# Kernel optimization log

Hardware: AMD Instinct MI355X
Metric: run time of the kernel (lower is better)

## Reference

```python
import jax, jax.numpy as jnp
import numpy as np

N_NODES = 20000
IN_CH = 7
HID = 256
HEADS = 8
NEG_SLOPE = 0.2


def glorot(key, shape):
    fan = shape[0] + shape[-1] if len(shape) == 2 else int(np.prod(shape))
    lim = jnp.sqrt(6.0 / fan)
    return jax.random.uniform(key, shape, jnp.float32, -lim, lim)


def setup_inputs() -> dict:
    key = jax.random.key(0)
    ks = jax.random.split(key, 12)
    x = jax.random.normal(ks[0], (N_NODES, IN_CH), jnp.float32)
    edge_index = jax.random.randint(ks[1], (2, 160000), 0, N_NODES, jnp.int64)
    # conv1: in=7 -> heads=8, out=256, concat
    W1 = glorot(ks[2], (IN_CH, HEADS * HID))
    att_src1 = glorot(ks[3], (HEADS, HID))
    att_dst1 = glorot(ks[4], (HEADS, HID))
    b1 = jnp.zeros((HEADS * HID,), jnp.float32)
    # conv2: in=2048 -> heads=1, out=256, mean (concat=False)
    W2 = glorot(ks[5], (HEADS * HID, 1 * HID))
    att_src2 = glorot(ks[6], (1, HID))
    att_dst2 = glorot(ks[7], (1, HID))
    b2 = jnp.zeros((HID,), jnp.float32)
    return {"x": x, "edge_index": edge_index, "W1": W1, "att_src1": att_src1,
            "att_dst1": att_dst1, "b1": b1, "W2": W2, "att_src2": att_src2,
            "att_dst2": att_dst2, "b2": b2}


def gat_conv(x, src, dst, W, att_src, att_dst, bias, concat):
    # PyG GATConv (eval mode, dropout disabled)
    H, C = att_src.shape
    n = x.shape[0]
    h = (x @ W).reshape(n, H, C)                      # [N,H,C]
    a_src = jnp.sum(h * att_src[None], axis=-1)       # [N,H]
    a_dst = jnp.sum(h * att_dst[None], axis=-1)       # [N,H]
    alpha = a_src[src] + a_dst[dst]                   # [E,H]
    alpha = jax.nn.leaky_relu(alpha, NEG_SLOPE)
    # segment softmax over incoming edges of each destination node
    amax = jax.ops.segment_max(alpha, dst, num_segments=n)
    alpha = jnp.exp(alpha - amax[dst])
    denom = jax.ops.segment_sum(alpha, dst, num_segments=n)
    alpha = alpha / (denom[dst] + 1e-16)
    msg = h[src] * alpha[:, :, None]                  # [E,H,C] gather + weight
    out = jax.ops.segment_sum(msg, dst, num_segments=n)  # scatter-add aggregate
    out = out.reshape(n, H * C) if concat else out.mean(axis=1)
    return out + bias


def reference(x, edge_index, W1, att_src1, att_dst1, b1, W2, att_src2, att_dst2, b2):
    n = x.shape[0]
    # PyG GATConv default: add self-loops
    loops = jnp.arange(n, dtype=edge_index.dtype)
    src = jnp.concatenate([edge_index[0], loops])
    dst = jnp.concatenate([edge_index[1], loops])
    h = gat_conv(x, src, dst, W1, att_src1, att_dst1, b1, concat=True)
    h = jax.nn.elu(h)
    out = gat_conv(h, src, dst, W2, att_src2, att_dst2, b2, concat=False)
    return out
```

## Files before the change

kernel.cpp:

```cpp
#include <hip/hip_runtime.h>
#include <hip/hip_bf16.h>

#define N_NODES 20000
#define E_ORIG  160000
#define E_TOT   180000
#define HEADS   8
#define HID     256
#define F1      2048
#define NEG     0.2f
#define MAXDEG  96
#define GBKS    32
#define BMG     80

typedef __attribute__((ext_vector_type(8))) short  short8;
typedef __attribute__((ext_vector_type(4))) short  short4_;
typedef __attribute__((ext_vector_type(4))) float  f32x4;

__device__ inline float bf2f(ushort u){ union{unsigned u32; float f;} v; v.u32=((unsigned)u)<<16; return v.f; }
__device__ inline ushort f2bf(float f){
  union{float f; unsigned u;} v; v.f=f;
  unsigned lsb=(v.u>>16)&1u; v.u += 0x7fffu + lsb; return (ushort)(v.u>>16);
}

__device__ inline void gload16(const ushort* g, ushort* s){
  __builtin_amdgcn_global_load_lds((const __attribute__((address_space(1))) unsigned int*)g,
                                   (__attribute__((address_space(3))) unsigned int*)s, 16, 0, 0);
}

__global__ __launch_bounds__(256) void k_pre(const float* __restrict__ x, const float* __restrict__ W1,
    const float* __restrict__ as1, const float* __restrict__ ad1, const float* __restrict__ W2,
    float* __restrict__ a_src1, float* __restrict__ a_dst1, ushort* __restrict__ W2bT,
    int* __restrict__ cnt){
  __shared__ float s_w[128];
  __shared__ ushort sh[256][65];
  int tid = threadIdx.x, bid = blockIdx.x;
  if (tid < 128){
    int t = tid & 63;
    int k = t>>3, i = t&7;
    float v = 0.f;
    if (i < 7){
      const float* wp = W1 + i*F1 + (k<<8);
      const float* ap = ((tid<64) ? as1 : ad1) + (k<<8);
      f32x4 a4 = {0,0,0,0};
      for (int c=0;c<256;c+=4)
        a4 += (*(const f32x4*)&wp[c]) * (*(const f32x4*)&ap[c]);
      v = a4[0]+a4[1]+a4[2]+a4[3];
    }
    s_w[tid] = v;
  }
  __syncthreads();
  {
    int nl = tid>>3, k = tid&7;
    int n = bid*32 + nl;
    if (n < N_NODES){
      float s=0.f, d=0.f;
      const float* ws = &s_w[k*8];
      const float* wd = &s_w[64+k*8];
#pragma unroll
      for (int i=0;i<7;i++){
        float xv = x[n*7+i];
        s += xv*ws[i]; d += xv*wd[i];
      }
      a_src1[n*8+k]=s; a_dst1[n*8+k]=d;
    }
  }
  if (bid >= 32 && bid < 111){
    int i = (bid-32)*256 + tid;
    if (i < N_NODES) cnt[i] = 0;
  }
  if (bid < 32){
    int k0 = bid*64;
    for (int kk=0; kk<64; kk++) sh[tid][kk] = f2bf(W2[(size_t)(k0+kk)*256 + tid]);
    __syncthreads();
#pragma unroll
    for (int c8=0; c8<8; c8++){
      short8 v;
#pragma unroll
      for (int j=0;j<8;j++) v[j] = (short)sh[tid][c8*8+j];
      *(short8*)&W2bT[(size_t)tid*F1 + k0 + c8*8] = v;
    }
  }
}

__global__ void k_scat(const int* __restrict__ ei, int* __restrict__ cnt, int* __restrict__ bucket){
  int e = blockIdx.x*256 + threadIdx.x;
  if (e >= E_TOT) return;
  int s, d;
  if (e < E_ORIG){ s = ei[e]; d = ei[E_ORIG + e]; }
  else           { s = d = e - E_ORIG; }
  int pos = atomicAdd(&cnt[d], 1);
  if (pos < MAXDEG) bucket[d*MAXDEG + pos] = s;
}

__global__ __launch_bounds__(512) void k_sa1(const int* __restrict__ cnt, const int* __restrict__ bucket,
    const float* __restrict__ a_src1, const float* __restrict__ a_dst1,
    const float* __restrict__ x, const float* __restrict__ W1, const float* __restrict__ b1,
    ushort* __restrict__ x2){
  __shared__ float sxa[8][64];
  int tid = threadIdx.x, wv = tid>>6, lane = tid&63;
  int n = blockIdx.x*8 + wv;
  {
    int k = lane>>3, i = lane&7;
    int ie = (i==7)?0:i;
    int base = n*MAXDEG;
    int deg  = cnt[n]; if (deg>MAXDEG) deg=MAXDEG;
    float ad = a_dst1[n*8+k];
    int src0 = (lane<deg)    ? bucket[base+lane]    : 0;
    int src1 = (lane+64<deg) ? bucket[base+lane+64] : 0;
    float denom = 0.f, acc = 0.f;
    int j = 0;
    for (; j+2<=deg; j+=2){
      int s0 = (j<64)   ? __shfl(src0,j)     : __shfl(src1,j-64);
      int s1 = (j+1<64) ? __shfl(src0,j+1)   : __shfl(src1,j-63);
      float A0 = a_src1[(size_t)s0*8+k] + ad;
      float A1 = a_src1[(size_t)s1*8+k] + ad;
      float X0 = x[(size_t)s0*7+ie];
      float X1 = x[(size_t)s1*7+ie];
      A0 = (A0>0.f)?A0:NEG*A0;  A1 = (A1>0.f)?A1:NEG*A1;
      float w0 = __expf(A0),   w1 = __expf(A1);
      denom += w0; acc += w0*X0;
      denom += w1; acc += w1*X1;
    }
    if (j<deg){
      int s0 = (j<64) ? __shfl(src0,j) : __shfl(src1,j-64);
      float A0 = a_src1[(size_t)s0*8+k] + ad;
      A0 = (A0>0.f)?A0:NEG*A0;
      float w0 = __expf(A0);
      denom += w0; acc += w0*x[(size_t)s0*7+ie];
    }
    sxa[wv][lane] = acc/denom;
  }
  __syncthreads();
  int kh = tid>>6, c4 = (tid&63)<<2;
  f32x4 w1r[7];
#pragma unroll
  for (int i=0;i<7;i++) w1r[i] = *(const f32x4*)(W1 + i*F1 + (kh<<8) + c4);
  f32x4 bb = *(const f32x4*)(b1 + (kh<<8) + c4);
#pragma unroll
  for (int g=0; g<8; g++){
    int nn = blockIdx.x*8 + g;
    const float* xa = &sxa[g][kh<<3];
    f32x4 h = bb;
#pragma unroll
    for (int i=0;i<7;i++) h += xa[i]*w1r[i];
    short4_ o;
#pragma unroll
    for (int j=0;j<4;j++){ float v=h[j]; v=(v>0.f)?v:(__expf(v)-1.f); o[j]=(short)f2bf(v); }
    *(short4_*)(x2 + (size_t)nn*F1 + (kh<<8) + c4) = o;
  }
}

__global__ __launch_bounds__(256) void k_gemm2m(const ushort* __restrict__ A,
    const ushort* __restrict__ BT, ushort* __restrict__ h2b,
    const float* __restrict__ as2, const float* __restrict__ ad2,
    float* __restrict__ a_src2, float* __restrict__ a_dst2){
  __shared__ __align__(16) ushort S[2][(BMG+256)*64];
  int tid = threadIdx.x;
  int m0 = blockIdx.x*BMG;
  int w = tid>>6, l = tid&63;
  int lrow = l&15, lk = l>>4;
  int nc = w<<6;

  const ushort* gp[11];
#pragma unroll
  for (int rep=0;rep<11;rep++){
    int lin = rep*256 + tid;
    if (lin < BMG*8){
      int r = lin>>3, s = lin&7;
      gp[rep] = A + (size_t)(m0+r)*F1 + ((s ^ (r&7))<<3);
    } else if (lin < (BMG+256)*8){
      int j = lin - BMG*8;
      int c = j>>3, s = j&7;
      gp[rep] = BT + (size_t)c*F1 + ((s ^ (c&7))<<3);
    } else gp[rep] = BT;
  }

  f32x4 acc[5][4] = {};

#pragma unroll
  for (int rep=0;rep<10;rep++) gload16(gp[rep], &S[0][(rep*256+tid)<<3]);
  if (tid < 128) gload16(gp[10], &S[0][(10*256+tid)<<3]);
  __syncthreads();

  int cur = 0;
  for (int t=0; t<GBKS; t++){
    if (t+1 < GBKS){
      int k0 = (t+1)<<6;
#pragma unroll
      for (int rep=0;rep<10;rep++) gload16(gp[rep]+k0, &S[cur^1][(rep*256+tid)<<3]);
      if (tid < 128) gload16(gp[10]+k0, &S[cur^1][(10*256+tid)<<3]);
    }
    const ushort* as_ = &S[cur][0];
    const ushort* bs_ = &S[cur][BMG*64];
#pragma unroll
    for (int kk=0;kk<2;kk++){
      short8 af[5], bfr[4];
#pragma unroll
      for (int m=0;m<5;m++){
        int r = (m<<4) + lrow;
        af[m] = *(const short8*)&as_[(r<<6) + ((((kk<<2)|lk) ^ (r&7))<<3)];
      }
#pragma unroll
      for (int n=0;n<4;n++){
        int c = nc + (n<<4) + lrow;
        bfr[n] = *(const short8*)&bs_[(c<<6) + ((((kk<<2)|lk) ^ (c&7))<<3)];
      }
#pragma unroll
      for (int m=0;m<5;m++)
#pragma unroll
        for (int n=0;n<4;n++)
          acc[m][n] = __builtin_amdgcn_mfma_f32_16x16x32_bf16(af[m], bfr[n], acc[m][n], 0,0,0);
    }
    __syncthreads();
    cur ^= 1;
  }

  float* sps = (float*)&S[0][0];
  float* spd = sps + BMG*4;
  float s2v[4], d2v[4];
#pragma unroll
  for (int n=0;n<4;n++){
    int col = nc + (n<<4) + lrow;
    s2v[n]=as2[col]; d2v[n]=ad2[col];
  }
#pragma unroll
  for (int m=0;m<5;m++){
#pragma unroll
    for (int j=0;j<4;j++){
      int lr = (m<<4) + (lk<<2) + j;
      int grow = m0 + lr;
      float ps=0.f, pd=0.f;
#pragma unroll
      for (int n=0;n<4;n++){
        float v = acc[m][n][j];
        ps += v*s2v[n]; pd += v*d2v[n];
        h2b[(size_t)grow*256 + nc+(n<<4)+lrow] = f2bf(v);
      }
      ps += __shfl_xor(ps,8); ps += __shfl_xor(ps,4); ps += __shfl_xor(ps,2); ps += __shfl_xor(ps,1);
      pd += __shfl_xor(pd,8); pd += __shfl_xor(pd,4); pd += __shfl_xor(pd,2); pd += __shfl_xor(pd,1);
      if (lrow==0){
        sps[(lr<<2) | w] = ps;
        spd[(lr<<2) | w] = pd;
      }
    }
  }
  __syncthreads();
  if (tid < BMG){
    int grow = m0 + tid;
    f32x4 a = *(const f32x4*)&sps[tid<<2];
    f32x4 b = *(const f32x4*)&spd[tid<<2];
    a_src2[grow] = a[0]+a[1]+a[2]+a[3];
    a_dst2[grow] = b[0]+b[1]+b[2]+b[3];
  }
}

__global__ __launch_bounds__(256) void k_agg2(const int* __restrict__ cnt, const int* __restrict__ bucket,
    const float* __restrict__ a_src2, const float* __restrict__ a_dst2, const ushort* __restrict__ h2b,
    const float* __restrict__ b2, float* __restrict__ out){
  int tid = threadIdx.x, wv = tid>>6, lane = tid&63;
  int n = blockIdx.x*4 + wv;
  int base = n*MAXDEG;
  int deg  = cnt[n]; if (deg > MAXDEG) deg = MAXDEG;
  float ad = a_dst2[n];

  int src0 = (lane<deg)     ? bucket[base+lane]    : 0;
  int src1 = (lane+64<deg)  ? bucket[base+lane+64] : 0;
  float a0 = -1e30f, a1 = -1e30f;
  if (lane<deg)   { float a = a_src2[src0]+ad; a0 = (a>0.f)?a:NEG*a; }
  if (lane+64<deg){ float a = a_src2[src1]+ad; a1 = (a>0.f)?a:NEG*a; }
  float m = fmaxf(a0,a1);
  for (int off=32; off; off>>=1) m = fmaxf(m, __shfl_xor(m,off));
  float e0 = (lane<deg)    ? __expf(a0-m) : 0.f;
  float e1 = (lane+64<deg) ? __expf(a1-m) : 0.f;
  float s = e0+e1;
  for (int off=32; off; off>>=1) s += __shfl_xor(s,off);
  float inv = 1.f/(s+1e-16f);
  e0 *= inv; e1 *= inv;

  int c0 = lane<<2;
  float acc0=0.f, acc1=0.f, acc2=0.f, acc3=0.f;
  int d1 = (deg<64)?deg:64;
  for (int j=0;j<d1;j++){
    float w = __shfl(e0, j);
    int  sj = __shfl(src0, j);
    short4_ hv = *(const short4_*)(h2b + (size_t)sj*256 + c0);
    acc0 += w*bf2f((ushort)hv[0]); acc1 += w*bf2f((ushort)hv[1]);
    acc2 += w*bf2f((ushort)hv[2]); acc3 += w*bf2f((ushort)hv[3]);
  }
  for (int j=64;j<deg;j++){
    float w = __shfl(e1, j-64);
    int  sj = __shfl(src1, j-64);
    short4_ hv = *(const short4_*)(h2b + (size_t)sj*256 + c0);
    acc0 += w*bf2f((ushort)hv[0]); acc1 += w*bf2f((ushort)hv[1]);
    acc2 += w*bf2f((ushort)hv[2]); acc3 += w*bf2f((ushort)hv[3]);
  }
  f32x4 bb = *(const f32x4*)(b2 + c0);
  f32x4 o; o[0]=acc0+bb[0]; o[1]=acc1+bb[1]; o[2]=acc2+bb[2]; o[3]=acc3+bb[3];
  *(f32x4*)(out + (size_t)n*256 + c0) = o;
}

extern "C" void kernel_launch(void* const* d_in, const int* in_sizes, int n_in,
                              void* d_out, int out_size, void* d_ws, size_t ws_size,
                              hipStream_t stream){
  const float* x      = (const float*)d_in[0];
  const int*   ei     = (const int*)  d_in[1];
  const float* W1     = (const float*)d_in[2];
  const float* att_s1 = (const float*)d_in[3];
  const float* att_d1 = (const float*)d_in[4];
  const float* b1     = (const float*)d_in[5];
  const float* W2     = (const float*)d_in[6];
  const float* att_s2 = (const float*)d_in[7];
  const float* att_d2 = (const float*)d_in[8];
  const float* b2     = (const float*)d_in[9];
  float* out = (float*)d_out;

  char* p = (char*)d_ws;
  auto alloc = [&](size_t bytes)->char*{ char* r = p; p += (bytes + 255) & ~(size_t)255; return r; };
  ushort* x2    = (ushort*)alloc((size_t)N_NODES*F1*2);
  ushort* W2bT  = (ushort*)alloc((size_t)F1*256*2);
  ushort* h2b   = (ushort*)alloc((size_t)N_NODES*256*2);
  float*  a_src1= (float*) alloc((size_t)N_NODES*8*4);
  float*  a_dst1= (float*) alloc((size_t)N_NODES*8*4);
  float*  a_src2= (float*) alloc((size_t)N_NODES*4);
  float*  a_dst2= (float*) alloc((size_t)N_NODES*4);
  int*    cnt   = (int*)   alloc((size_t)N_NODES*4);
  int*    bucket= (int*)   alloc((size_t)N_NODES*MAXDEG*4);

  k_pre    <<<(N_NODES+31)/32, 256, 0, stream>>>(x, W1, att_s1, att_d1, W2,
                                                 a_src1, a_dst1, W2bT, cnt);
  k_scat   <<<(E_TOT+255)/256, 256, 0, stream>>>(ei, cnt, bucket);
  k_sa1    <<<N_NODES/8, 512, 0, stream>>>(cnt, bucket, a_src1, a_dst1, x, W1, b1, x2);
  k_gemm2m <<<N_NODES/BMG, 256, 0, stream>>>(x2, W2bT, h2b, att_s2, att_d2, a_src2, a_dst2);
  k_agg2   <<<N_NODES/4, 256, 0, stream>>>(cnt, bucket, a_src2, a_dst2, h2b, b2, out);
}
```

Before: 120.1 us.

## Triple-buffer LDS stages in GEMM2 with vmcnt-based waits instead of syncthreads

Converts the second-layer GEMM K-loop from double to triple LDS buffering, prefetching two stages ahead and waiting with explicit vmcnt counts plus raw barriers rather than full __syncthreads. Idle threads issue dummy loads into a scratch buffer so every thread issues the same number of loads per stage, keeping the vmcnt count uniform. The aim is to hide global load latency behind MFMA work, at the cost of more LDS per block and possibly lower occupancy.

Result: slower. 133.8 us (+11.4%).

```diff
diff --git a/kernel.cpp b/kernel.cpp
--- a/kernel.cpp
+++ b/kernel.cpp
@@ -154,7 +154,8 @@
     const ushort* __restrict__ BT, ushort* __restrict__ h2b,
     const float* __restrict__ as2, const float* __restrict__ ad2,
     float* __restrict__ a_src2, float* __restrict__ a_dst2){
-  __shared__ __align__(16) ushort S[2][(BMG+256)*64];
+  __shared__ __align__(16) ushort S[3][(BMG+256)*64];
+  __shared__ __align__(16) ushort scr[128*8];
   int tid = threadIdx.x;
   int m0 = blockIdx.x*BMG;
   int w = tid>>6, l = tid&63;
@@ -163,35 +164,49 @@
 
   const ushort* gp[11];
 #pragma unroll
-  for (int rep=0;rep<11;rep++){
+  for (int rep=0;rep<10;rep++){
     int lin = rep*256 + tid;
     if (lin < BMG*8){
       int r = lin>>3, s = lin&7;
       gp[rep] = A + (size_t)(m0+r)*F1 + ((s ^ (r&7))<<3);
-    } else if (lin < (BMG+256)*8){
+    } else {
       int j = lin - BMG*8;
       int c = j>>3, s = j&7;
       gp[rep] = BT + (size_t)c*F1 + ((s ^ (c&7))<<3);
-    } else gp[rep] = BT;
-  }
+    }
+  }
+  {
+    int lin = 10*256 + tid;
+    if (lin < (BMG+256)*8){
+      int j = lin - BMG*8;
+      int c = j>>3, s = j&7;
+      gp[10] = BT + (size_t)c*F1 + ((s ^ (c&7))<<3);
+    } else {
+      gp[10] = BT + ((size_t)(tid&63))*8;
+    }
+  }
+
+  auto STAGE = [&](int t, int b){
+    int k0 = t<<6;
+#pragma unroll
+    for (int rep=0;rep<10;rep++) gload16(gp[rep]+k0, &S[b][(rep*256+tid)<<3]);
+    ushort* d = (tid<128) ? &S[b][(10*256+tid)<<3] : &scr[(tid-128)<<3];
+    gload16(gp[10]+k0, d);
+  };
 
   f32x4 acc[5][4] = {};
 
-#pragma unroll
-  for (int rep=0;rep<10;rep++) gload16(gp[rep], &S[0][(rep*256+tid)<<3]);
-  if (tid < 128) gload16(gp[10], &S[0][(10*256+tid)<<3]);
-  __syncthreads();
-
-  int cur = 0;
+  STAGE(0,0);
+  STAGE(1,1);
+  asm volatile("s_waitcnt vmcnt(11)" ::: "memory");
+  __builtin_amdgcn_s_barrier();
+  __builtin_amdgcn_sched_barrier(0);
+
+  int c0=0, c1=1, c2=2;
   for (int t=0; t<GBKS; t++){
-    if (t+1 < GBKS){
-      int k0 = (t+1)<<6;
-#pragma unroll
-      for (int rep=0;rep<10;rep++) gload16(gp[rep]+k0, &S[cur^1][(rep*256+tid)<<3]);
-      if (tid < 128) gload16(gp[10]+k0, &S[cur^1][(10*256+tid)<<3]);
-    }
-    const ushort* as_ = &S[cur][0];
-    const ushort* bs_ = &S[cur][BMG*64];
+    if (t+2 < GBKS) STAGE(t+2, c2);
+    const ushort* as_ = &S[c0][0];
+    const ushort* bs_ = &S[c0][BMG*64];
 #pragma unroll
     for (int kk=0;kk<2;kk++){
       short8 af[5], bfr[4];
@@ -211,8 +226,13 @@
         for (int n=0;n<4;n++)
           acc[m][n] = __builtin_amdgcn_mfma_f32_16x16x32_bf16(af[m], bfr[n], acc[m][n], 0,0,0);
     }
-    __syncthreads();
-    cur ^= 1;
+    if (t+1 < GBKS){
+      if (t+2 < GBKS) asm volatile("s_waitcnt vmcnt(11)" ::: "memory");
+      else            asm volatile("s_waitcnt vmcnt(0)"  ::: "memory");
+      __builtin_amdgcn_s_barrier();
+      __builtin_amdgcn_sched_barrier(0);
+    }
+    int tmp=c0; c0=c1; c1=c2; c2=tmp;
   }
 
   float* sps = (float*)&S[0][0];
```
